# Kernel optimization log

Hardware: AMD Instinct MI355X
Metric: run time of the kernel (lower is better)

The kernel has to match this reference:

```python
import jax, jax.numpy as jnp
import numpy as np

E = 23  # unique experts
K = 3   # activated experts per token


def setup_inputs() -> dict:
    key = jax.random.key(0)
    ks = jax.random.split(key, 8)
    B, S, D, H = 4, 1024, 1024, 768
    sd = 1.0 / np.sqrt(D)
    sh = 1.0 / np.sqrt(H)
    return {
        "x": jax.random.normal(ks[0], (B, S, D), jnp.float32),
        "gate_W": jax.random.normal(ks[1], (D, E), jnp.float32) * sd,
        "gate_b": jnp.zeros((E,), jnp.float32),
        "route_bias": jnp.zeros((E,), jnp.float32),  # registered buffer 'bias'
        "W1": jax.random.normal(ks[2], (E, D, H), jnp.float32) * sd,
        "b1": jnp.zeros((E, H), jnp.float32),
        "W2": jax.random.normal(ks[3], (E, H, D), jnp.float32) * sh,
        "b2": jnp.zeros((E, D), jnp.float32),
        "sW1": jax.random.normal(ks[4], (D, H), jnp.float32) * sd,
        "sb1": jnp.zeros((H,), jnp.float32),
        "sW2": jax.random.normal(ks[5], (H, D), jnp.float32) * sh,
        "sb2": jnp.zeros((D,), jnp.float32),
    }


def _gelu(x):
    return jax.nn.gelu(x, approximate=False)  # torch nn.GELU default = exact erf


def reference(x, gate_W, gate_b, route_bias, W1, b1, W2, b2, sW1, sb1, sW2, sb2):
    o_shape = x.shape
    xt = x.reshape(-1, o_shape[-1])                       # [N, D]
    N = xt.shape[0]
    gate_weights = jax.nn.sigmoid(xt @ gate_W + gate_b)   # [N, E]
    _, top_idx = jax.lax.top_k(gate_weights + route_bias, K)  # [N, K]
    top_w = jnp.take_along_axis(gate_weights, top_idx, axis=-1)
    top_w = top_w / top_w.sum(axis=-1, keepdims=True)     # [N, K]
    onehot = jax.nn.one_hot(top_idx, E, dtype=xt.dtype)   # [N, K, E]
    combine = jnp.einsum('nke,nk->ne', onehot, top_w)     # [N, E] routed weights
    counts = onehot.sum(axis=(0, 1))                      # tokens per expert
    # dense-equivalent grouped expert MLPs (same math as gather/split/concat)
    h = _gelu(jnp.einsum('nd,edh->enh', xt, W1) + b1[:, None, :])   # [E, N, H]
    y = jnp.einsum('enh,ehd->end', h, W2) + b2[:, None, :]          # [E, N, D]
    routed = jnp.einsum('end,ne->nd', y, combine)
    shared = _gelu(xt @ sW1 + sb1) @ sW2 + sb2
    out = shared + routed
    # aux load-balance loss
    gw_norm = gate_weights / gate_weights.sum(axis=-1, keepdims=True)
    P = gw_norm.mean(axis=0)
    Fvec = (E * counts) / (K * N)
    aux_loss = (P * Fvec).sum()
    return out.reshape(o_shape), aux_loss
```

## Files before the change

kernel.cpp:

```cpp
#include <hip/hip_runtime.h>
#include <hip/hip_bf16.h>
#include <stdint.h>

#define N_TOK 4096
#define DDIM  1024
#define HDIM  768
#define NEXP  23
#define TOPK  3
#define MAXTILE 152
#define SLOTS   19456

typedef float floatx4 __attribute__((ext_vector_type(4)));
typedef short short8  __attribute__((ext_vector_type(8)));

__device__ __forceinline__ short f2bf(float f) {
    __hip_bfloat16 h = __float2bfloat16(f);
    return *reinterpret_cast<short*>(&h);
}
__device__ __forceinline__ float bf2f(short s) {
    unsigned u = ((unsigned)(unsigned short)s) << 16;
    return __uint_as_float(u);
}
__device__ __forceinline__ float gelu_erf(float v) {
    return 0.5f * v * (1.0f + erff(v * 0.70710678118654752f));
}
__device__ __forceinline__ void gl_lds16(const short* g, short* l) {
    __builtin_amdgcn_global_load_lds(
        (const __attribute__((address_space(1))) void*)g,
        (__attribute__((address_space(3))) void*)l, 16, 0, 0);
}

#define PREP_GATE   1024
#define PREP_XCVT   N_TOK
#define PREP_BIAS   168
#define PREP_TCVT   9216
#define PREP_GRID   (PREP_GATE + PREP_XCVT + PREP_BIAS + PREP_TCVT)

__global__ __launch_bounds__(256) void prep_kernel(
    const float* __restrict__ x, const float* __restrict__ gate_W,
    const float* __restrict__ gate_b, const float* __restrict__ route_bias,
    int* __restrict__ top_idx, float* __restrict__ top_w,
    float* __restrict__ psum_part, short* __restrict__ xb,
    const float* __restrict__ b1, const float* __restrict__ sb1,
    const float* __restrict__ b2, const float* __restrict__ sb2,
    float* __restrict__ bias1_all, float* __restrict__ bias2_all,
    const float* __restrict__ W1, const float* __restrict__ sW1, short* __restrict__ W1T,
    const float* __restrict__ W2, const float* __restrict__ sW2, short* __restrict__ W2T)
{
    __shared__ float ldsbuf[2304];
    const int b = blockIdx.x;
    if (b >= PREP_GATE) {
        const int bb = b - PREP_GATE;
        if (bb < PREP_XCVT) {
            size_t i = (size_t)bb * 256 + threadIdx.x;
            float4 v = ((const float4*)x)[i];
            short4 o;
            o.x = f2bf(v.x); o.y = f2bf(v.y); o.z = f2bf(v.z); o.w = f2bf(v.w);
            ((short4*)xb)[i] = o;
        } else if (bb < PREP_XCVT + PREP_BIAS) {
            int i = (bb - PREP_XCVT) * 256 + threadIdx.x;
            if (i < 24 * HDIM) {
                bias1_all[i] = (i < NEXP * HDIM) ? b1[i] : sb1[i - NEXP * HDIM];
            } else {
                int j = i - 24 * HDIM;
                if (j < 24 * DDIM)
                    bias2_all[j] = (j < NEXP * DDIM) ? b2[j] : sb2[j - NEXP * DDIM];
            }
        } else {
            int idx = bb - (PREP_XCVT + PREP_BIAS);
            const float* s; short* d; int R, C, cx, cy;
            if (idx < 24 * 192) {
                const int w = idx / 192, rem = idx % 192;
                R = DDIM; C = HDIM; cx = rem % 12; cy = rem / 12;
                s = (w < NEXP) ? W1 + (size_t)w * DDIM * HDIM : sW1;
                d = W1T + (size_t)w * DDIM * HDIM;
            } else {
                idx -= 24 * 192;
                const int w = idx / 192, rem = idx % 192;
                R = HDIM; C = DDIM; cx = rem % 16; cy = rem / 16;
                s = (w < NEXP) ? W2 + (size_t)w * HDIM * DDIM : sW2;
                d = W2T + (size_t)w * HDIM * DDIM;
            }
            const int c0 = cx * 64, r0 = cy * 64;
            const int t = threadIdx.x;
            short (*tile)[72] = (short(*)[72])ldsbuf;

            const int rr = t >> 4, cc = (t & 15) << 2;
#pragma unroll
            for (int i = 0; i < 64; i += 16) {
                float4 v = *(const float4*)&s[(size_t)(r0 + i + rr) * C + c0 + cc];
                tile[cc + 0][i + rr] = f2bf(v.x);
                tile[cc + 1][i + rr] = f2bf(v.y);
                tile[cc + 2][i + rr] = f2bf(v.z);
                tile[cc + 3][i + rr] = f2bf(v.w);
            }
            __syncthreads();
            const int cc2 = t >> 3, rr2 = (t & 7) << 3;
#pragma unroll
            for (int j = 0; j < 64; j += 32) {
                *(short8*)&d[(size_t)(c0 + j + cc2) * R + r0 + rr2] =
                    *(const short8*)&tile[j + cc2][rr2];
            }
        }
        return;
    }
    const int wave = threadIdx.x >> 6, lane = threadIdx.x & 63;
    const int n = b * 4 + wave;

    float (*gw)[25]  = (float(*)[25])ldsbuf;
    float (*ps)[NEXP] = (float(*)[NEXP])(ldsbuf + 1600);

    float acc[NEXP];
#pragma unroll
    for (int e = 0; e < NEXP; e++) acc[e] = 0.f;

    const float* xr = x + (size_t)n * DDIM;
    for (int c0 = 0; c0 < DDIM; c0 += 64) {
        for (int idx = threadIdx.x; idx < 64 * NEXP; idx += 256)
            gw[idx / NEXP][idx % NEXP] = gate_W[(size_t)c0 * NEXP + idx];
        __syncthreads();
        float xd = xr[c0 + lane];
#pragma unroll
        for (int e = 0; e < NEXP; e++) acc[e] += xd * gw[lane][e];
        __syncthreads();
    }
    for (int off = 32; off > 0; off >>= 1) {
#pragma unroll
        for (int e = 0; e < NEXP; e++) acc[e] += __shfl_xor(acc[e], off, 64);
    }

    float p[NEXP], s = 0.f;
#pragma unroll
    for (int e = 0; e < NEXP; e++) {
        p[e] = 1.f / (1.f + expf(-(acc[e] + gate_b[e])));
        s += p[e];
    }
    const float inv = 1.f / s;

    if (lane == 0) {
#pragma unroll
        for (int e = 0; e < NEXP; e++) ps[wave][e] = p[e] * inv;
        int idx[TOPK]; float w[TOPK]; bool used[NEXP] = {};
        for (int k = 0; k < TOPK; k++) {
            float best = -1e30f; int bi = 0;
            for (int e = 0; e < NEXP; e++) {
                if (!used[e]) {
                    float sc = p[e] + route_bias[e];
                    if (sc > best) { best = sc; bi = e; }
                }
            }
            used[bi] = true; idx[k] = bi; w[k] = p[bi];
        }
        float wsum = w[0] + w[1] + w[2];
        for (int k = 0; k < TOPK; k++) {
            top_idx[n * TOPK + k] = idx[k];
            top_w[n * TOPK + k]   = w[k] / wsum;
        }
    }
    __syncthreads();
    if (threadIdx.x < NEXP) {
        int e = threadIdx.x;
        psum_part[(size_t)b * NEXP + e] =
            ps[0][e] + ps[1][e] + ps[2][e] + ps[3][e];
    }
}

__global__ __launch_bounds__(256) void plan_kernel(
    const int* __restrict__ top_idx, const float* __restrict__ psum_part,
    int* __restrict__ tile_e, int* __restrict__ tok_of_slot,
    int* __restrict__ slot_of_tok, float* __restrict__ out_aux)
{
    __shared__ int   cnt[NEXP];
    __shared__ float psum[NEXP];
    __shared__ int   tbase[NEXP + 1];
    __shared__ int   lcur[NEXP];
    const int t = threadIdx.x;
    if (t < NEXP) { cnt[t] = 0; psum[t] = 0.f; lcur[t] = 0; }
    __syncthreads();

    for (int i = t; i < N_TOK * TOPK; i += 256)
        atomicAdd(&cnt[top_idx[i]], 1);

    float loc[NEXP];
#pragma unroll
    for (int e = 0; e < NEXP; e++) loc[e] = 0.f;
    for (int b = t; b < N_TOK / 4; b += 256) {
        const float* row = psum_part + (size_t)b * NEXP;
#pragma unroll
        for (int e = 0; e < NEXP; e++) loc[e] += row[e];
    }
#pragma unroll
    for (int e = 0; e < NEXP; e++) atomicAdd(&psum[e], loc[e]);
    __syncthreads();

    if (t == 0) {
        int tb = 0; float aux = 0.f;
        for (int e = 0; e < NEXP; e++) {
            tbase[e] = tb;
            float P = psum[e] / (float)N_TOK;
            float F = (float)NEXP * (float)cnt[e] / ((float)TOPK * (float)N_TOK);
            aux += P * F;
            tb += (cnt[e] + 127) >> 7;
        }
        tbase[NEXP] = tb;
        *out_aux = aux;
    }
    __syncthreads();
    const int tr = tbase[NEXP];
    const int P  = tr << 7;
    for (int i = t; i < MAXTILE; i += 256) {
        int v = -1;
        if (i < tr) {
            for (int e = 0; e < NEXP; e++)
                if (i >= tbase[e] && i < tbase[e + 1]) v = e;
        } else if (i < tr + N_TOK / 128) v = NEXP;
        tile_e[i] = v;
    }
    for (int i = t; i < N_TOK * TOPK; i += 256) {
        const int e = top_idx[i];
        const int pos = atomicAdd(&lcur[e], 1);
        const int slot = (tbase[e] << 7) + pos;
        const int n = i / 3, k = i - n * 3;
        tok_of_slot[slot] = n;
        slot_of_tok[n * 4 + k] = slot;
    }
    for (int n = t; n < N_TOK; n += 256) {
        tok_of_slot[P + n] = n;
        slot_of_tok[n * 4 + 3] = P + n;
    }
}

template <bool FFN1>
__global__ __launch_bounds__(256) void gemm_kernel(
    const short* __restrict__ Abase, const int* __restrict__ tok_of_slot,
    const int* __restrict__ tile_e, const short* __restrict__ Wall,
    const float* __restrict__ bias_all, short* __restrict__ outb)
{
    constexpr int KD = FFN1 ? DDIM : HDIM;
    constexpr int NC = FFN1 ? HDIM : DDIM;
    constexpr int KI = KD / 32;
    constexpr int GX = NC / 128;
    constexpr int NWG = GX * MAXTILE;
    constexpr int Q = NWG / 8, RM = NWG % 8;

    int bid = blockIdx.y * GX + blockIdx.x;
    {
        const int xcd = bid & 7, off = bid >> 3;
        bid = (xcd < RM) ? (xcd * (Q + 1) + off)
                         : (RM * (Q + 1) + (xcd - RM) * Q + off);
    }
    const int tile = bid / GX;
    const int e = tile_e[tile];
    if (e < 0) return;
    const int slot0 = tile * 128;
    const int n0 = (bid - tile * GX) * 128;

    __shared__ short smem[3 * 4096 * 2];
    short* const As = smem;
    short* const Bs = smem + 3 * 4096;

    const int t = threadIdx.x;
    const int w = t >> 6, l = t & 63;
    const int quad = l >> 4, l16 = l & 15;
    const int wr = w >> 1, wc = w & 1;

    const int ra0 = w * 32 + (l >> 2);
    const int ra1 = ra0 + 16;
    const int ko  = (l & 3) << 3;

    const short *ap0, *ap1;
    if constexpr (FFN1) {
        int t0 = tok_of_slot[slot0 + ra0];
        int t1 = tok_of_slot[slot0 + ra1];
        t0 = ((unsigned)t0 < (unsigned)N_TOK) ? t0 : 0;
        t1 = ((unsigned)t1 < (unsigned)N_TOK) ? t1 : 0;
        ap0 = Abase + (size_t)t0 * KD + ko;
        ap1 = Abase + (size_t)t1 * KD + ko;
    } else {
        ap0 = Abase + (size_t)(slot0 + ra0) * KD + ko;
        ap1 = Abase + (size_t)(slot0 + ra1) * KD + ko;
    }
    const short* bbase = Wall + (size_t)e * NC * KD + (size_t)n0 * KD;
    const short* bp0 = bbase + (size_t)ra0 * KD + ko;
    const short* bp1 = bbase + (size_t)ra1 * KD + ko;

    const int ldo0 = (w * 32) * 32;
    const int ldo1 = (w * 32 + 16) * 32;

    floatx4 acc[4][4] = {};

#pragma unroll
    for (int p = 0; p < 3; p++) {
        gl_lds16(ap0, As + p * 4096 + ldo0); gl_lds16(ap1, As + p * 4096 + ldo1);
        gl_lds16(bp0, Bs + p * 4096 + ldo0); gl_lds16(bp1, Bs + p * 4096 + ldo1);
        ap0 += 32; ap1 += 32; bp0 += 32; bp1 += 32;
    }

#pragma unroll
    for (int k = 0; k < KI; k++) {
        if (k < KI - 2)       asm volatile("s_waitcnt vmcnt(8)" ::: "memory");
        else if (k == KI - 2) asm volatile("s_waitcnt vmcnt(4)" ::: "memory");
        else                  asm volatile("s_waitcnt vmcnt(0)" ::: "memory");
        asm volatile("s_barrier" ::: "memory");

        const int s = k % 3;
        short8 af[4], bf[4];
#pragma unroll
        for (int i = 0; i < 4; i++)
            af[i] = *(const short8*)(As + s * 4096 + (wr * 64 + i * 16 + l16) * 32 + quad * 8);
#pragma unroll
        for (int j = 0; j < 4; j++)
            bf[j] = *(const short8*)(Bs + s * 4096 + (wc * 64 + j * 16 + l16) * 32 + quad * 8);
#pragma unroll
        for (int i = 0; i < 4; i++)
#pragma unroll
            for (int j = 0; j < 4; j++)
                acc[i][j] = __builtin_amdgcn_mfma_f32_16x16x32_bf16(af[i], bf[j], acc[i][j], 0, 0, 0);

        asm volatile("s_waitcnt lgkmcnt(0)" ::: "memory");
        asm volatile("s_barrier" ::: "memory");
        if (k + 3 < KI) {
            gl_lds16(ap0, As + s * 4096 + ldo0); gl_lds16(ap1, As + s * 4096 + ldo1);
            gl_lds16(bp0, Bs + s * 4096 + ldo0); gl_lds16(bp1, Bs + s * 4096 + ldo1);
            ap0 += 32; ap1 += 32; bp0 += 32; bp1 += 32;
        }
    }

    short* const OT = smem;
    const int bias_off = e * NC + n0;
#pragma unroll
    for (int j = 0; j < 4; j++) {
        const int colL = wc * 64 + j * 16 + l16;
        const float bv = bias_all[bias_off + colL];
        const int cg = colL >> 3, wi = colL & 7;
#pragma unroll
        for (int i = 0; i < 4; i++)
#pragma unroll
            for (int r = 0; r < 4; r++) {
                const int rowL = wr * 64 + i * 16 + quad * 4 + r;
                float v = acc[i][j][r] + bv;
                if constexpr (FFN1) v = gelu_erf(v);
                OT[rowL * 128 + (((cg ^ ((rowL >> 2) & 3)) << 3) | wi)] = f2bf(v);
            }
    }
    __syncthreads();
#pragma unroll
    for (int p = 0; p < 8; p++) {
        const int rowL = p * 16 + (t >> 4);
        const int g = t & 15;
        const short8 v = *(const short8*)(OT + rowL * 128 + ((g ^ ((rowL >> 2) & 3)) << 3));
        *(short8*)&outb[(size_t)(slot0 + rowL) * NC + n0 + g * 8] = v;
    }
}

__global__ __launch_bounds__(256) void combine_kernel(
    const short* __restrict__ ybuf, const int* __restrict__ slot_of_tok,
    const float* __restrict__ top_w, float* __restrict__ out)
{
    const int n = blockIdx.x;
    const int c = threadIdx.x;
    const int s0 = slot_of_tok[n * 4 + 0];
    const int s1 = slot_of_tok[n * 4 + 1];
    const int s2 = slot_of_tok[n * 4 + 2];
    const int ss = slot_of_tok[n * 4 + 3];
    const float w0 = top_w[n * 3 + 0];
    const float w1 = top_w[n * 3 + 1];
    const float w2 = top_w[n * 3 + 2];

    short4 y0 = ((const short4*)(ybuf + (size_t)s0 * DDIM))[c];
    short4 y1 = ((const short4*)(ybuf + (size_t)s1 * DDIM))[c];
    short4 y2 = ((const short4*)(ybuf + (size_t)s2 * DDIM))[c];
    short4 ys = ((const short4*)(ybuf + (size_t)ss * DDIM))[c];

    float4 o;
    o.x = bf2f(ys.x) + w0 * bf2f(y0.x) + w1 * bf2f(y1.x) + w2 * bf2f(y2.x);
    o.y = bf2f(ys.y) + w0 * bf2f(y0.y) + w1 * bf2f(y1.y) + w2 * bf2f(y2.y);
    o.z = bf2f(ys.z) + w0 * bf2f(y0.z) + w1 * bf2f(y1.z) + w2 * bf2f(y2.z);
    o.w = bf2f(ys.w) + w0 * bf2f(y0.w) + w1 * bf2f(y1.w) + w2 * bf2f(y2.w);
    ((float4*)(out + (size_t)n * DDIM))[c] = o;
}

extern "C" void kernel_launch(void* const* d_in, const int* in_sizes, int n_in,
                              void* d_out, int out_size, void* d_ws, size_t ws_size,
                              hipStream_t stream)
{
    const float* x          = (const float*)d_in[0];
    const float* gate_W     = (const float*)d_in[1];
    const float* gate_b     = (const float*)d_in[2];
    const float* route_bias = (const float*)d_in[3];
    const float* W1         = (const float*)d_in[4];
    const float* b1         = (const float*)d_in[5];
    const float* W2         = (const float*)d_in[6];
    const float* b2         = (const float*)d_in[7];
    const float* sW1        = (const float*)d_in[8];
    const float* sb1        = (const float*)d_in[9];
    const float* sW2        = (const float*)d_in[10];
    const float* sb2        = (const float*)d_in[11];
    float* out = (float*)d_out;

    uint8_t* ws = (uint8_t*)d_ws;
    int*   top_idx   = (int*)(ws);
    float* top_w     = (float*)(ws + 49152);
    int*   tile_e    = (int*)(ws + 98688);
    float* psum_part = (float*)(ws + 99328);
    int*   tok_slot  = (int*)(ws + 193536);
    int*   slot_tok  = (int*)(ws + 271360);
    float* bias1_all = (float*)(ws + 336896);
    float* bias2_all = (float*)(ws + 410624);
    short* xb        = (short*)(ws + 512000);
    short* W1T       = (short*)(ws + 8902656);
    short* W2T       = (short*)(ws + 46651392);
    short* hbuf      = (short*)(ws + 84400128);
    short* ybuf      = (short*)(ws + 512000);

    prep_kernel<<<PREP_GRID, 256, 0, stream>>>(
        x, gate_W, gate_b, route_bias, top_idx, top_w, psum_part,
        xb, b1, sb1, b2, sb2, bias1_all, bias2_all,
        W1, sW1, W1T, W2, sW2, W2T);
    plan_kernel<<<1, 256, 0, stream>>>(top_idx, psum_part, tile_e,
                                       tok_slot, slot_tok,
                                       out + (size_t)N_TOK * DDIM);

    gemm_kernel<true><<<dim3(HDIM / 128, MAXTILE), 256, 0, stream>>>(
        xb, tok_slot, tile_e, W1T, bias1_all, hbuf);
    gemm_kernel<false><<<dim3(DDIM / 128, MAXTILE), 256, 0, stream>>>(
        hbuf, tok_slot, tile_e, W2T, bias2_all, ybuf);
    combine_kernel<<<N_TOK, 256, 0, stream>>>(ybuf, slot_tok, top_w, out);
}
```

Measured before the change: 412.4 us.

## Fuse fp32 weight transpose-convert into GEMM B-tile loading, drop prep transpose pass

```diff
diff --git a/kernel.cpp b/kernel.cpp
--- a/kernel.cpp
+++ b/kernel.cpp
@@ -33,8 +33,7 @@
 #define PREP_GATE   1024
 #define PREP_XCVT   N_TOK
 #define PREP_BIAS   168
-#define PREP_TCVT   9216
-#define PREP_GRID   (PREP_GATE + PREP_XCVT + PREP_BIAS + PREP_TCVT)
+#define PREP_GRID   (PREP_GATE + PREP_XCVT + PREP_BIAS)
 
 __global__ __launch_bounds__(256) void prep_kernel(
     const float* __restrict__ x, const float* __restrict__ gate_W,
@@ -43,11 +42,9 @@
     float* __restrict__ psum_part, short* __restrict__ xb,
     const float* __restrict__ b1, const float* __restrict__ sb1,
     const float* __restrict__ b2, const float* __restrict__ sb2,
-    float* __restrict__ bias1_all, float* __restrict__ bias2_all,
-    const float* __restrict__ W1, const float* __restrict__ sW1, short* __restrict__ W1T,
-    const float* __restrict__ W2, const float* __restrict__ sW2, short* __restrict__ W2T)
+    float* __restrict__ bias1_all, float* __restrict__ bias2_all)
 {
-    __shared__ float ldsbuf[2304];
+    __shared__ float ldsbuf[1728];
     const int b = blockIdx.x;
     if (b >= PREP_GATE) {
         const int bb = b - PREP_GATE;
@@ -57,7 +54,7 @@
             short4 o;
             o.x = f2bf(v.x); o.y = f2bf(v.y); o.z = f2bf(v.z); o.w = f2bf(v.w);
             ((short4*)xb)[i] = o;
-        } else if (bb < PREP_XCVT + PREP_BIAS) {
+        } else {
             int i = (bb - PREP_XCVT) * 256 + threadIdx.x;
             if (i < 24 * HDIM) {
                 bias1_all[i] = (i < NEXP * HDIM) ? b1[i] : sb1[i - NEXP * HDIM];
@@ -66,48 +63,13 @@
                 if (j < 24 * DDIM)
                     bias2_all[j] = (j < NEXP * DDIM) ? b2[j] : sb2[j - NEXP * DDIM];
             }
-        } else {
-            int idx = bb - (PREP_XCVT + PREP_BIAS);
-            const float* s; short* d; int R, C, cx, cy;
-            if (idx < 24 * 192) {
-                const int w = idx / 192, rem = idx % 192;
-                R = DDIM; C = HDIM; cx = rem % 12; cy = rem / 12;
-                s = (w < NEXP) ? W1 + (size_t)w * DDIM * HDIM : sW1;
-                d = W1T + (size_t)w * DDIM * HDIM;
-            } else {
-                idx -= 24 * 192;
-                const int w = idx / 192, rem = idx % 192;
-                R = HDIM; C = DDIM; cx = rem % 16; cy = rem / 16;
-                s = (w < NEXP) ? W2 + (size_t)w * HDIM * DDIM : sW2;
-                d = W2T + (size_t)w * HDIM * DDIM;
-            }
-            const int c0 = cx * 64, r0 = cy * 64;
-            const int t = threadIdx.x;
-            short (*tile)[72] = (short(*)[72])ldsbuf;
-
-            const int rr = t >> 4, cc = (t & 15) << 2;
-#pragma unroll
-            for (int i = 0; i < 64; i += 16) {
-                float4 v = *(const float4*)&s[(size_t)(r0 + i + rr) * C + c0 + cc];
-                tile[cc + 0][i + rr] = f2bf(v.x);
-                tile[cc + 1][i + rr] = f2bf(v.y);
-                tile[cc + 2][i + rr] = f2bf(v.z);
-                tile[cc + 3][i + rr] = f2bf(v.w);
-            }
-            __syncthreads();
-            const int cc2 = t >> 3, rr2 = (t & 7) << 3;
-#pragma unroll
-            for (int j = 0; j < 64; j += 32) {
-                *(short8*)&d[(size_t)(c0 + j + cc2) * R + r0 + rr2] =
-                    *(const short8*)&tile[j + cc2][rr2];
-            }
         }
         return;
     }
     const int wave = threadIdx.x >> 6, lane = threadIdx.x & 63;
     const int n = b * 4 + wave;
 
-    float (*gw)[25]  = (float(*)[25])ldsbuf;
+    float (*gw)[25]   = (float(*)[25])ldsbuf;
     float (*ps)[NEXP] = (float(*)[NEXP])(ldsbuf + 1600);
 
     float acc[NEXP];
@@ -233,8 +195,9 @@
 template <bool FFN1>
 __global__ __launch_bounds__(256) void gemm_kernel(
     const short* __restrict__ Abase, const int* __restrict__ tok_of_slot,
-    const int* __restrict__ tile_e, const short* __restrict__ Wall,
-    const float* __restrict__ bias_all, short* __restrict__ outb)
+    const int* __restrict__ tile_e, const float* __restrict__ Wfp,
+    const float* __restrict__ Wsh, const float* __restrict__ bias_all,
+    short* __restrict__ outb)
 {
     constexpr int KD = FFN1 ? DDIM : HDIM;
     constexpr int NC = FFN1 ? HDIM : DDIM;
@@ -266,7 +229,7 @@
 
     const int ra0 = w * 32 + (l >> 2);
     const int ra1 = ra0 + 16;
-    const int ko  = (l & 3) << 3;
+    const int ko  = (((l & 3) ^ ((l >> 4) & 3)) << 3);
 
     const short *ap0, *ap1;
     if constexpr (FFN1) {
@@ -280,37 +243,66 @@
         ap0 = Abase + (size_t)(slot0 + ra0) * KD + ko;
         ap1 = Abase + (size_t)(slot0 + ra1) * KD + ko;
     }
-    const short* bbase = Wall + (size_t)e * NC * KD + (size_t)n0 * KD;
-    const short* bp0 = bbase + (size_t)ra0 * KD + ko;
-    const short* bp1 = bbase + (size_t)ra1 * KD + ko;
-
     const int ldo0 = (w * 32) * 32;
     const int ldo1 = (w * 32 + 16) * 32;
 
+    const int nB = t >> 1;
+    const int q0 = (t & 1) * 2;
+    const int swzB = ((t >> 3) & 3) << 4;
+    const float* wsrc = (e < NEXP) ? Wfp + (size_t)e * KD * NC : Wsh;
+    const float* wp = wsrc + (size_t)(q0 * 8) * NC + (n0 + nB);
+
+    const int rsw = ((l16 >> 2) & 3) << 4;
+
+    float rA[16], rB[16];
     floatx4 acc[4][4] = {};
 
-#pragma unroll
-    for (int p = 0; p < 3; p++) {
-        gl_lds16(ap0, As + p * 4096 + ldo0); gl_lds16(ap1, As + p * 4096 + ldo1);
-        gl_lds16(bp0, Bs + p * 4096 + ldo0); gl_lds16(bp1, Bs + p * 4096 + ldo1);
-        ap0 += 32; ap1 += 32; bp0 += 32; bp1 += 32;
-    }
+    auto fillA = [&](int slot) {
+        gl_lds16(ap0, As + slot * 4096 + ldo0);
+        gl_lds16(ap1, As + slot * 4096 + ldo1);
+        ap0 += 32; ap1 += 32;
+    };
+    auto loadB = [&](float (&r)[16]) {
+#pragma unroll
+        for (int j = 0; j < 16; j++) r[j] = wp[(size_t)j * NC];
+        wp += (size_t)32 * NC;
+    };
+    auto writeB = [&](float (&r)[16], int slot) {
+        char* bb = (char*)(Bs + slot * 4096) + nB * 64;
+        short8 u0, u1;
+#pragma unroll
+        for (int i = 0; i < 8; i++) { u0[i] = f2bf(r[i]); u1[i] = f2bf(r[8 + i]); }
+        *(short8*)(bb + (((q0 + 0) * 16) ^ swzB)) = u0;
+        *(short8*)(bb + (((q0 + 1) * 16) ^ swzB)) = u1;
+    };
+
+    fillA(0); loadB(rA);
+    fillA(1); loadB(rB);
+    asm volatile("s_waitcnt vmcnt(18)" ::: "memory");
+    writeB(rA, 0);
+    fillA(2); loadB(rA);
 
 #pragma unroll
     for (int k = 0; k < KI; k++) {
-        if (k < KI - 2)       asm volatile("s_waitcnt vmcnt(8)" ::: "memory");
-        else if (k == KI - 2) asm volatile("s_waitcnt vmcnt(4)" ::: "memory");
-        else                  asm volatile("s_waitcnt vmcnt(0)" ::: "memory");
+        if (k < KI - 2) asm volatile("s_waitcnt vmcnt(18)" ::: "memory");
+        else            asm volatile("s_waitcnt vmcnt(0)" ::: "memory");
+        if (k + 1 < KI) {
+            if ((k + 1) & 1) writeB(rB, (k + 1) % 3);
+            else             writeB(rA, (k + 1) % 3);
+        }
+        asm volatile("s_waitcnt lgkmcnt(0)" ::: "memory");
         asm volatile("s_barrier" ::: "memory");
 
         const int s = k % 3;
         short8 af[4], bf[4];
 #pragma unroll
         for (int i = 0; i < 4; i++)
-            af[i] = *(const short8*)(As + s * 4096 + (wr * 64 + i * 16 + l16) * 32 + quad * 8);
+            af[i] = *(const short8*)((const char*)(As + s * 4096)
+                     + (wr * 64 + i * 16 + l16) * 64 + ((quad * 16) ^ rsw));
 #pragma unroll
         for (int j = 0; j < 4; j++)
-            bf[j] = *(const short8*)(Bs + s * 4096 + (wc * 64 + j * 16 + l16) * 32 + quad * 8);
+            bf[j] = *(const short8*)((const char*)(Bs + s * 4096)
+                     + (wc * 64 + j * 16 + l16) * 64 + ((quad * 16) ^ rsw));
 #pragma unroll
         for (int i = 0; i < 4; i++)
 #pragma unroll
@@ -320,9 +312,9 @@
         asm volatile("s_waitcnt lgkmcnt(0)" ::: "memory");
         asm volatile("s_barrier" ::: "memory");
         if (k + 3 < KI) {
-            gl_lds16(ap0, As + s * 4096 + ldo0); gl_lds16(ap1, As + s * 4096 + ldo1);
-            gl_lds16(bp0, Bs + s * 4096 + ldo0); gl_lds16(bp1, Bs + s * 4096 + ldo1);
-            ap0 += 32; ap1 += 32; bp0 += 32; bp1 += 32;
+            fillA(s);
+            if ((k + 3) & 1) loadB(rB);
+            else             loadB(rA);
         }
     }
 
@@ -408,22 +400,19 @@
     float* bias1_all = (float*)(ws + 336896);
     float* bias2_all = (float*)(ws + 410624);
     short* xb        = (short*)(ws + 512000);
-    short* W1T       = (short*)(ws + 8902656);
-    short* W2T       = (short*)(ws + 46651392);
-    short* hbuf      = (short*)(ws + 84400128);
-    short* ybuf      = (short*)(ws + 512000);
+    short* hbuf      = (short*)(ws + 8900608);
+    short* ybuf      = (short*)(ws + 38785024);
 
     prep_kernel<<<PREP_GRID, 256, 0, stream>>>(
         x, gate_W, gate_b, route_bias, top_idx, top_w, psum_part,
-        xb, b1, sb1, b2, sb2, bias1_all, bias2_all,
-        W1, sW1, W1T, W2, sW2, W2T);
+        xb, b1, sb1, b2, sb2, bias1_all, bias2_all);
     plan_kernel<<<1, 256, 0, stream>>>(top_idx, psum_part, tile_e,
                                        tok_slot, slot_tok,
                                        out + (size_t)N_TOK * DDIM);
 
     gemm_kernel<true><<<dim3(HDIM / 128, MAXTILE), 256, 0, stream>>>(
-        xb, tok_slot, tile_e, W1T, bias1_all, hbuf);
+        xb, tok_slot, tile_e, W1, sW1, bias1_all, hbuf);
     gemm_kernel<false><<<dim3(DDIM / 128, MAXTILE), 256, 0, stream>>>(
-        hbuf, tok_slot, tile_e, W2T, bias2_all, ybuf);
+        hbuf, tok_slot, tile_e, W2, sW2, bias2_all, ybuf);
     combine_kernel<<<N_TOK, 256, 0, stream>>>(ybuf, slot_tok, top_w, out);
 }
```

After: 514.6 us. 24.8% more time.
